# Kernel tuning notes

Measured on AMD Instinct MI355X. Metric: run time of the kernel, lower is better.

The kernel has to match this reference:

```python
import jax, jax.numpy as jnp
import numpy as np

IN_F, OUT_F, LAT, RES, K, B = 512, 512, 512, 64, 3, 8
EPS = 1e-08
C_LIN = 1.0 / np.sqrt(LAT)          # EqualizedWeight scale for linear
C_CONV = 1.0 / np.sqrt(IN_F * K * K)  # EqualizedWeight scale for conv


def setup_inputs() -> dict:
    key = jax.random.key(0)
    k1, k2, k3, k4 = jax.random.split(key, 4)
    return {
        "x": jax.random.normal(k1, (B, IN_F, RES, RES), dtype=jnp.float32),
        "latent": jax.random.normal(k2, (B, LAT), dtype=jnp.float32),
        "w_lin": jax.random.normal(k3, (IN_F, LAT), dtype=jnp.float32),
        "b_lin": jnp.ones((IN_F,), dtype=jnp.float32),
        "w_conv": jax.random.normal(k4, (OUT_F, IN_F, K, K), dtype=jnp.float32),
        "b_conv": jnp.zeros((OUT_F,), dtype=jnp.float32),
    }


def reference(x, latent, w_lin, b_lin, w_conv, b_conv):
    # EqualizedLinear: s = latent @ (w_lin*c).T + b_lin*lr_mul  -> [B, IN_F]
    s = latent @ (w_lin * C_LIN).T + b_lin
    # ModulatedConv2d. Per-sample weight w[b,o,i,k,k] = (w_conv*c)[o,i,k,k]*s[b,i],
    # demodulated by sigma_inv[b,o] = rsqrt(sum_{i,k,k} w^2 + eps).
    w = w_conv * C_CONV  # [O, I, K, K]
    # sum_{k,k} w^2 over spatial -> [O, I], then contract with s^2 -> [B, O]
    w2 = jnp.sum(w * w, axis=(2, 3))  # [O, I]
    sigma_inv = jax.lax.rsqrt(jnp.einsum('oi,bi->bo', w2, s * s) + EPS)
    # conv(x, w*s_b) == conv(x * s_b, w): modulate input, single batched conv,
    # then demodulate output per (b, o). Avoids materializing B*O filters.
    x_mod = x * s[:, :, None, None]
    y = jax.lax.conv_general_dilated(
        x_mod, w,
        window_strides=(1, 1),
        padding=[((K - 1) // 2, (K - 1) // 2)] * 2,
        dimension_numbers=('NCHW', 'OIHW', 'NCHW'),
    )
    y = y * sigma_inv[:, :, None, None] + b_conv[None, :, None, None]
    return y
```

## Files before the change

### kernel.cpp

```cpp
#include <hip/hip_runtime.h>
#include <hip/hip_bf16.h>

#define IN_F 512
#define OUT_F 512
#define LATD 512
#define RES 64
#define BATCH 8
#define EPSV 1e-8f

static constexpr float C_LIN  = 0.04419417382415922f;
static constexpr float C_CONV = 0.014731391274719739f;

typedef __attribute__((ext_vector_type(8)))  short short8;
typedef __attribute__((ext_vector_type(16))) float f32x16;

union BF { __hip_bfloat16 h; short s; };

__device__ __forceinline__ void async_load16(const char* g, char* l) {
  __builtin_amdgcn_global_load_lds(
      (const __attribute__((address_space(1))) unsigned int*)g,
      (__attribute__((address_space(3))) unsigned int*)l, 16, 0, 0);
}

__global__ void k_prep(const float* __restrict__ w_conv,
                       short* __restrict__ wb,
                       float* __restrict__ w2,
                       char* __restrict__ xmp,
                       const float* __restrict__ latent,
                       const float* __restrict__ w_lin,
                       const float* __restrict__ b_lin,
                       float* __restrict__ s) {
  const int t = blockIdx.x * 256 + threadIdx.x;
  {
    const int o = t >> 9;
    const int i = t & 511;
    const float* src = w_conv + (size_t)t * 9;
    const int c = i >> 4, hf0 = (i >> 3) & 1, ch = i & 7;
    const int ob = o >> 7, ol = o & 127;
    short* dst = wb + (size_t)(c * 4 + ob) * 18432 + hf0 * 1024 + ol * 8 + ch;
    float sum = 0.f;
#pragma unroll
    for (int tap = 0; tap < 9; ++tap) {
      const float v = src[tap] * C_CONV;
      sum += v * v;
      BF cv; cv.h = __float2bfloat16(v);
      dst[tap * 2048] = cv.s;
    }
    w2[t] = sum;
  }

  if (blockIdx.x < 256) {
    char* base = xmp + (size_t)blockIdx.x * 139392;
    for (int q = threadIdx.x; q < 520; q += 256) {
      int h, hf, w;
      if (q < 132)      { h = 0;  hf = (q >= 66) ? 1 : 0; w = q - hf * 66; }
      else if (q < 264) { const int r = q - 132; h = 65; hf = (r >= 66) ? 1 : 0; w = r - hf * 66; }
      else              { const int r = q - 264; h = (r >> 2) + 1; hf = (r >> 1) & 1; w = (r & 1) * 65; }
      *(uint4*)(base + ((size_t)(h * 132 + hf * 66 + w)) * 16) = make_uint4(0u, 0u, 0u, 0u);
    }
  }

  if (blockIdx.x < 128) {
    const int wv = threadIdx.x >> 6, lane = threadIdx.x & 63;
    const int i = blockIdx.x * 4 + wv;
    const float4* wl = (const float4*)(w_lin + (size_t)i * LATD);
    const float4 w0 = wl[lane * 2], w1 = wl[lane * 2 + 1];
    float acc[BATCH];
#pragma unroll
    for (int b = 0; b < BATCH; ++b) {
      const float4* lt = (const float4*)(latent + (size_t)b * LATD);
      const float4 l0 = lt[lane * 2], l1 = lt[lane * 2 + 1];
      acc[b] = w0.x * l0.x + w0.y * l0.y + w0.z * l0.z + w0.w * l0.w +
               w1.x * l1.x + w1.y * l1.y + w1.z * l1.z + w1.w * l1.w;
    }
#pragma unroll
    for (int b = 0; b < BATCH; ++b) {
      float v = acc[b];
#pragma unroll
      for (int off = 32; off > 0; off >>= 1) v += __shfl_down(v, off);
      if (lane == 0) s[b * IN_F + i] = v * C_LIN + b_lin[i];
    }
  }
}

__global__ void k_mod_sigma(const float* __restrict__ x,
                            const float* __restrict__ s,
                            char* __restrict__ xmp,
                            const float* __restrict__ w2,
                            float* __restrict__ sigma_inv) {
  if (blockIdx.x < 128) {
    const int o = blockIdx.x * 4 + (threadIdx.x >> 6);
    const int lane = threadIdx.x & 63;
    float acc[BATCH];
#pragma unroll
    for (int b = 0; b < BATCH; ++b) acc[b] = 0.f;
#pragma unroll
    for (int k = 0; k < 8; ++k) {
      const int i = k * 64 + lane;
      const float w = w2[o * IN_F + i];
#pragma unroll
      for (int b = 0; b < BATCH; ++b) {
        const float sv = s[b * IN_F + i];
        acc[b] += w * sv * sv;
      }
    }
#pragma unroll
    for (int b = 0; b < BATCH; ++b) {
      float v = acc[b];
#pragma unroll
      for (int off = 32; off > 0; off >>= 1) v += __shfl_down(v, off);
      if (lane == 0) sigma_inv[b * OUT_F + o] = rsqrtf(v + EPSV);
    }
    return;
  }
  const int bid  = blockIdx.x - 128;
  const int h    = bid & 63;
  const int ic32 = (bid >> 6) & 15;
  const int b    = bid >> 10;
  __shared__ float tile[32][65];
  const int tid = threadIdx.x;
  {
    const int il = tid >> 3, w8 = (tid & 7) * 8;
    const int i = ic32 * 32 + il;
    const float sv = s[b * IN_F + i];
    const float* xp = x + (((size_t)(b * IN_F + i) * RES + h) * RES + w8);
    const float4 v0 = *(const float4*)xp;
    const float4 v1 = *(const float4*)(xp + 4);
    tile[il][w8 + 0] = v0.x * sv; tile[il][w8 + 1] = v0.y * sv;
    tile[il][w8 + 2] = v0.z * sv; tile[il][w8 + 3] = v0.w * sv;
    tile[il][w8 + 4] = v1.x * sv; tile[il][w8 + 5] = v1.y * sv;
    tile[il][w8 + 6] = v1.z * sv; tile[il][w8 + 7] = v1.w * sv;
  }
  __syncthreads();
  {
    const int w = tid >> 2, part = tid & 3;
    const int chalf = part >> 1, hf = part & 1;
    short8 pk;
#pragma unroll
    for (int j = 0; j < 8; ++j) {
      BF cv; cv.h = __float2bfloat16(tile[chalf * 16 + hf * 8 + j][w]);
      pk[j] = cv.s;
    }
    const int c = ic32 * 2 + chalf;
    char* dst = xmp + (size_t)(c * 8 + b) * 139392 +
                ((size_t)(h + 1) * 132 + hf * 66 + (w + 1)) * 16;
    *(short8*)dst = pk;
  }
}

__global__ __launch_bounds__(512, 2)
void k_conv(const char* __restrict__ xmp,
            const short* __restrict__ wbg,
            const float* __restrict__ sigma_inv,
            const float* __restrict__ b_conv,
            float* __restrict__ out) {
  __shared__ __align__(16) char lds[115968];
  const int l = blockIdx.x;
  const int ob = (l >> 3) & 3;
  const int b  = l & 7;
  const int h0 = (l >> 5) * 8;
  const int o0 = ob * 128;
  const int tid = threadIdx.x;
  const int wave = tid >> 6, lane = tid & 63;
  const int l31 = lane & 31, half = lane >> 5;
  const int oh = wave >> 2;
  const int q  = wave & 3;
  const int r0 = (q >> 1) * 4;
  const int c0 = (q & 1) * 32;

  f32x16 acc[2][4];
#pragma unroll
  for (int i = 0; i < 2; ++i)
#pragma unroll
    for (int j = 0; j < 4; ++j)
#pragma unroll
      for (int r = 0; r < 16; ++r) acc[i][j][r] = 0.f;

  const char* xsrc0 = xmp + (size_t)b * 139392 + (size_t)h0 * 2112;
  const char* wsrc0 = (const char*)wbg + (size_t)ob * 36864;

#pragma unroll
  for (int k = 0; k < 2; ++k) {
    const int j = tid + k * 512;
    async_load16(xsrc0 + j * 16, lds + j * 16);
  }
  if (tid < 296) { const int j = 1024 + tid; async_load16(xsrc0 + j * 16, lds + j * 16); }
#pragma unroll
  for (int k = 0; k < 4; ++k) {
    const int j = tid + k * 512;
    async_load16(wsrc0 + j * 16, lds + 42240 + j * 16);
  }
  if (tid < 256) { const int j = 2048 + tid; async_load16(wsrc0 + j * 16, lds + 42240 + j * 16); }
  __syncthreads();

  for (int ic = 0; ic < 32; ++ic) {
    const int p = ic & 1;
    if (ic + 1 < 32) {
      const char* xs  = xsrc0 + (size_t)(ic + 1) * (8 * 139392);
      const char* wsr = wsrc0 + (size_t)(ic + 1) * 147456;
      char* xd = lds + (p ^ 1) * 21120;
      char* wd = lds + 42240 + (p ^ 1) * 36864;
#pragma unroll
      for (int k = 0; k < 2; ++k) {
        const int j = tid + k * 512;
        async_load16(xs + j * 16, xd + j * 16);
      }
      if (tid < 296) { const int j = 1024 + tid; async_load16(xs + j * 16, xd + j * 16); }
#pragma unroll
      for (int k = 0; k < 4; ++k) {
        const int j = tid + k * 512;
        async_load16(wsr + j * 16, wd + j * 16);
      }
      if (tid < 256) { const int j = 2048 + tid; async_load16(wsr + j * 16, wd + j * 16); }
    }
    const char* xp = lds + p * 21120;
    const char* wp = lds + 42240 + p * 36864;
#pragma unroll
    for (int dw = 0; dw < 3; ++dw) {
      short8 brow[6];
#pragma unroll
      for (int rr = 0; rr < 6; ++rr)
        brow[rr] = *(const short8*)(
            xp + (((r0 + rr) * 132) + half * 66 + c0 + dw + l31) * 16);
#pragma unroll
      for (int dh = 0; dh < 3; ++dh) {
        const int tap = dh * 3 + dw;
        short8 a[2];
#pragma unroll
        for (int f = 0; f < 2; ++f)
          a[f] = *(const short8*)(
              wp + tap * 4096 + half * 2048 + (oh * 64 + f * 32 + l31) * 16);
        __builtin_amdgcn_s_setprio(1);
#pragma unroll
        for (int tpr = 0; tpr < 4; ++tpr)
#pragma unroll
          for (int f = 0; f < 2; ++f)
            acc[f][tpr] = __builtin_amdgcn_mfma_f32_32x32x16_bf16(
                a[f], brow[tpr + dh], acc[f][tpr], 0, 0, 0);
        __builtin_amdgcn_s_setprio(0);
      }
    }
    __syncthreads();
  }

#pragma unroll
  for (int f = 0; f < 2; ++f) {
#pragma unroll
    for (int g = 0; g < 4; ++g) {
#pragma unroll
      for (int r = 0; r < 4; ++r) {
        const int o = o0 + oh * 64 + f * 32 + r + 8 * g + 4 * half;
        const float sig  = sigma_inv[b * OUT_F + o];
        const float bias = b_conv[o];
        const int reg = g * 4 + r;
#pragma unroll
        for (int tpr = 0; tpr < 4; ++tpr) {
          const int h = h0 + r0 + tpr;
          const int w = c0 + l31;
          out[(((size_t)(b * OUT_F + o) * RES + h) * RES) + w] =
              acc[f][tpr][reg] * sig + bias;
        }
      }
    }
  }
}

extern "C" void kernel_launch(void* const* d_in, const int* in_sizes, int n_in,
                              void* d_out, int out_size, void* d_ws, size_t ws_size,
                              hipStream_t stream) {
  const float* x      = (const float*)d_in[0];
  const float* latent = (const float*)d_in[1];
  const float* w_lin  = (const float*)d_in[2];
  const float* b_lin  = (const float*)d_in[3];
  const float* w_conv = (const float*)d_in[4];
  const float* b_conv = (const float*)d_in[5];
  float* out = (float*)d_out;

  char* ws = (char*)d_ws;
  char*  xmp       = ws;
  short* wb        = (short*)(ws + 35684352);
  float* w2        = (float*)(ws + 40402944);
  float* s         = (float*)(ws + 41451520);
  float* sigma_inv = (float*)(ws + 41467904);

  k_prep<<<1024, 256, 0, stream>>>(w_conv, wb, w2, xmp, latent, w_lin, b_lin, s);
  k_mod_sigma<<<128 + BATCH * 16 * RES, 256, 0, stream>>>(x, s, xmp, w2, sigma_inv);
  k_conv<<<256, 512, 0, stream>>>(xmp, wb, sigma_inv, b_conv, out);
}
```

Before: 249.0 us.

## Prefetch weight fragments in conv loop and batch rows in modulation kernel

```diff
diff --git a/kernel.cpp b/kernel.cpp
--- a/kernel.cpp
+++ b/kernel.cpp
@@ -114,37 +114,44 @@
     return;
   }
   const int bid  = blockIdx.x - 128;
-  const int h    = bid & 63;
-  const int ic32 = (bid >> 6) & 15;
-  const int b    = bid >> 10;
+  const int h8   = bid & 7;
+  const int ic32 = (bid >> 3) & 15;
+  const int b    = bid >> 7;
   __shared__ float tile[32][65];
   const int tid = threadIdx.x;
-  {
-    const int il = tid >> 3, w8 = (tid & 7) * 8;
-    const int i = ic32 * 32 + il;
-    const float sv = s[b * IN_F + i];
-    const float* xp = x + (((size_t)(b * IN_F + i) * RES + h) * RES + w8);
-    const float4 v0 = *(const float4*)xp;
-    const float4 v1 = *(const float4*)(xp + 4);
+  const int il = tid >> 3, w8 = (tid & 7) * 8;
+  const int i  = ic32 * 32 + il;
+  const float sv = s[b * IN_F + i];
+  const float* xrow = x + (size_t)(b * IN_F + i) * (RES * RES) + w8;
+  const int w = tid >> 2, part = tid & 3;
+  const int chalf = part >> 1, hf = part & 1;
+  const int c = ic32 * 2 + chalf;
+  char* dstb = xmp + (size_t)(c * 8 + b) * 139392 + ((size_t)hf * 66 + (w + 1)) * 16;
+
+  float4 v0 = *(const float4*)(xrow + (size_t)(h8 * 8) * RES);
+  float4 v1 = *(const float4*)(xrow + (size_t)(h8 * 8) * RES + 4);
+#pragma unroll
+  for (int hh = 0; hh < 8; ++hh) {
+    const int h = h8 * 8 + hh;
     tile[il][w8 + 0] = v0.x * sv; tile[il][w8 + 1] = v0.y * sv;
     tile[il][w8 + 2] = v0.z * sv; tile[il][w8 + 3] = v0.w * sv;
     tile[il][w8 + 4] = v1.x * sv; tile[il][w8 + 5] = v1.y * sv;
     tile[il][w8 + 6] = v1.z * sv; tile[il][w8 + 7] = v1.w * sv;
-  }
-  __syncthreads();
-  {
-    const int w = tid >> 2, part = tid & 3;
-    const int chalf = part >> 1, hf = part & 1;
+    float4 n0, n1;
+    if (hh < 7) {
+      n0 = *(const float4*)(xrow + (size_t)(h + 1) * RES);
+      n1 = *(const float4*)(xrow + (size_t)(h + 1) * RES + 4);
+    }
+    __syncthreads();
     short8 pk;
 #pragma unroll
     for (int j = 0; j < 8; ++j) {
       BF cv; cv.h = __float2bfloat16(tile[chalf * 16 + hf * 8 + j][w]);
       pk[j] = cv.s;
     }
-    const int c = ic32 * 2 + chalf;
-    char* dst = xmp + (size_t)(c * 8 + b) * 139392 +
-                ((size_t)(h + 1) * 132 + hf * 66 + (w + 1)) * 16;
-    *(short8*)dst = pk;
+    *(short8*)(dstb + (size_t)(h + 1) * 2112) = pk;
+    __syncthreads();
+    v0 = n0; v1 = n1;
   }
 }
 
@@ -167,6 +174,8 @@
   const int q  = wave & 3;
   const int r0 = (q >> 1) * 4;
   const int c0 = (q & 1) * 32;
+  const int st = (wave >> 2) & 1;
+  const int dseq[3] = {st, st + 1, st ? 0 : 2};
 
   f32x16 acc[2][4];
 #pragma unroll
@@ -215,8 +224,16 @@
     }
     const char* xp = lds + p * 21120;
     const char* wp = lds + 42240 + p * 36864;
-#pragma unroll
-    for (int dw = 0; dw < 3; ++dw) {
+
+    short8 a_cur[2], a_nxt[2];
+#pragma unroll
+    for (int f = 0; f < 2; ++f)
+      a_cur[f] = *(const short8*)(
+          wp + dseq[0] * 4096 + half * 2048 + (oh * 64 + f * 32 + l31) * 16);
+
+#pragma unroll
+    for (int dwi = 0; dwi < 3; ++dwi) {
+      const int dw = dseq[dwi];
       short8 brow[6];
 #pragma unroll
       for (int rr = 0; rr < 6; ++rr)
@@ -224,20 +241,23 @@
             xp + (((r0 + rr) * 132) + half * 66 + c0 + dw + l31) * 16);
 #pragma unroll
       for (int dh = 0; dh < 3; ++dh) {
-        const int tap = dh * 3 + dw;
-        short8 a[2];
-#pragma unroll
-        for (int f = 0; f < 2; ++f)
-          a[f] = *(const short8*)(
-              wp + tap * 4096 + half * 2048 + (oh * 64 + f * 32 + l31) * 16);
+        if (!(dwi == 2 && dh == 2)) {
+          const int dh_n = (dh < 2) ? dh + 1 : 0;
+          const int dw_n = (dh < 2) ? dw : dseq[dwi + 1];
+#pragma unroll
+          for (int f = 0; f < 2; ++f)
+            a_nxt[f] = *(const short8*)(
+                wp + (dh_n * 3 + dw_n) * 4096 + half * 2048 + (oh * 64 + f * 32 + l31) * 16);
+        }
         __builtin_amdgcn_s_setprio(1);
 #pragma unroll
         for (int tpr = 0; tpr < 4; ++tpr)
 #pragma unroll
           for (int f = 0; f < 2; ++f)
             acc[f][tpr] = __builtin_amdgcn_mfma_f32_32x32x16_bf16(
-                a[f], brow[tpr + dh], acc[f][tpr], 0, 0, 0);
+                a_cur[f], brow[tpr + dh], acc[f][tpr], 0, 0, 0);
         __builtin_amdgcn_s_setprio(0);
+        a_cur[0] = a_nxt[0]; a_cur[1] = a_nxt[1];
       }
     }
     __syncthreads();
@@ -284,6 +304,6 @@
   float* sigma_inv = (float*)(ws + 41467904);
 
   k_prep<<<1024, 256, 0, stream>>>(w_conv, wb, w2, xmp, latent, w_lin, b_lin, s);
-  k_mod_sigma<<<128 + BATCH * 16 * RES, 256, 0, stream>>>(x, s, xmp, w2, sigma_inv);
+  k_mod_sigma<<<128 + 1024, 256, 0, stream>>>(x, s, xmp, w2, sigma_inv);
   k_conv<<<256, 512, 0, stream>>>(xmp, wb, sigma_inv, b_conv, out);
 }
```

Measured after the change: 246.7 us. About the same (-0.9%).
